# Optimization experiments

Hardware: AMD Instinct MI355X
Metric: run time of the kernel (lower is better)

## Reference

```python
import jax, jax.numpy as jnp
import numpy as np

B, T, C, D = 4, 2048, 48, 512
L = 16                    # transcript length per video (distinct labels)
K = 9                     # bdy_kernel
CS = 15                   # cs_kernel
N_TR = L - 1
N_CAND = 3 * N_TR         # candidate_mul * pt_num
WIN_LEN = int(T / L * 0.15)   # int(t / t_len * win_scale)
ALPHA, BETA, GAMMA, TEMP = 1.0, 1.0, 0.1, 0.1
LOG2 = float(np.log(2.0))

def _bdy_kernel():
    ker = np.zeros((K, K), np.float32)
    c = K // 2
    ker[:c, :c] = 1; ker[c:, c:] = 1
    ker[:c, c:] = -1; ker[c:, :c] = -1
    ker[c, c] = 0
    return jnp.asarray(ker)

BDY_KER = _bdy_kernel()

def bdy_score_fn(prob):
    # prob: [T, C]; sliding windows of size K over time (zero padded)
    c = K // 2
    pad = jnp.pad(prob, ((c, c), (0, 0)))
    win = pad[jnp.arange(T)[:, None] + jnp.arange(K)[None, :]]       # [T,K,C]
    p = win[:, :, None, :]                                           # [T,K,1,C]
    m = (p + win[:, None, :, :]) / 2                                 # [T,K,K,C]
    # torch F.kl_div((m+1e-32).log(), p) = p*(log p - log(m+1e-32)), xlogy(0)=0
    kl = jnp.sum(jnp.where(p > 0, p * (jnp.log(jnp.where(p > 0, p, 1.0)) - jnp.log(m + 1e-32)), 0.0), -1)
    js = (kl + jnp.swapaxes(kl, 1, 2)) / 2
    js = -(js / LOG2 * 2 - 1)                                        # [T,K,K]
    return jnp.mean(BDY_KER[None] * js, axis=(-1, -2))               # [T]

def dp(cls_score):
    # cls_score: [N_TR, N_CAND]; min-cost alignment DP, inner jj-loop vectorized
    cost = -cls_score
    n_tr, n_x = N_TR, N_CAND
    W = 2 * n_tr + 1
    col = jnp.arange(W)
    inf = jnp.float32(jnp.inf)
    tr_at = jnp.clip(col // 2, 0, n_tr - 1)
    even = (col % 2 == 0)
    ge2 = col >= 2

    def init_cols(ii):
        c0 = jnp.where(ii < n_x - n_tr, 0.0, inf)
        c1 = jnp.where(ii <= n_x - n_tr, cost[0, ii], inf)
        d1 = jnp.where(ii <= n_x - n_tr, 1, 0).astype(jnp.int32)
        return c0, c1, d1

    c0, c1, d1 = init_cols(0)
    row0 = jnp.full((W,), inf).at[0].set(c0).at[1].set(c1)
    dir0 = jnp.zeros((W,), jnp.int32).at[1].set(d1)

    def step(prev, ii):
        dm1 = jnp.concatenate([jnp.full((1,), inf), prev[:-1]])
        dm2 = jnp.concatenate([jnp.full((2,), inf), prev[:-2]])
        c_at = cost[:, ii][tr_at]
        even_val = jnp.minimum(prev, dm1)
        even_dir = jnp.where(prev < dm1, 0, 1).astype(jnp.int32)
        odd_val = c_at + jnp.minimum(dm1, dm2)
        odd_dir = jnp.where(dm1 < dm2, 1, 2).astype(jnp.int32)
        c0, c1, d1 = init_cols(ii)
        new = jnp.where(ge2, jnp.where(even, even_val, odd_val), inf)
        new = new.at[0].set(c0).at[1].set(c1)
        dirs = jnp.where(ge2, jnp.where(even, even_dir, odd_dir), 0).astype(jnp.int32)
        dirs = dirs.at[1].set(d1)
        return new, dirs

    last, dirs = jax.lax.scan(step, row0, jnp.arange(1, n_x))
    dir_mat = jnp.concatenate([dir0[None], dirs], 0)                 # [n_x, W]
    cur_j0 = jnp.where(last[2 * n_tr] < last[2 * n_tr - 1], 2 * n_tr, 2 * n_tr - 1).astype(jnp.int32)

    def bt(cur_j, x):
        ii, dir_row = x
        is_odd = (cur_j % 2) == 1
        out_idx = jnp.where(is_odd, cur_j // 2, jnp.int32(n_tr))     # n_tr = OOB -> dropped
        new_j = cur_j - dir_row[cur_j]
        return new_j, (out_idx, ii.astype(jnp.int32))

    _, (oi, ovals) = jax.lax.scan(bt, cur_j0, (jnp.arange(n_x), dir_mat), reverse=True)
    return jnp.zeros((n_tr,), jnp.int32).at[oi].set(ovals, mode='drop')

def detect(logit, tr):
    # logit: [T,C] (detached), tr: [L] ints -> boundary frame indices [N_TR]
    prob = jax.nn.softmax(logit, -1)
    score = bdy_score_fn(prob).at[0].set(-jnp.inf)
    backup = score
    pos = jnp.arange(T)

    def pick(s, _):
        i = jnp.argmax(s)
        return jnp.where(jnp.abs(pos - i) <= WIN_LEN, -jnp.inf, s), i

    _, cand = jax.lax.scan(pick, score, None, length=N_CAND)
    cand = jnp.sort(cand)                                            # [N_CAND]
    # class-transition score at candidate points
    cc = CS // 2
    pairs = jnp.pad(prob[:, tr], ((cc, cc), (0, 0)))                 # [T+2cc, L]
    win = pairs[cand[:, None] + jnp.arange(CS)[None, :]]             # [N_CAND, CS, L]
    first, second = win[:, :, :-1], win[:, :, 1:]
    k0 = jnp.where(jnp.arange(CS) < cc, 1.0, -1.0)[None, :, None]
    cls = jnp.sum(k0 * (first - second), axis=1) / (2 * CS)          # [N_CAND, N_TR]
    cls = cls.T + backup[cand][None, :]                              # [N_TR, N_CAND]
    return cand[dp(cls)]

def _forward(tok_logit, fr_logit, vid_multi_hot, feat, mask, transcript):
    y = vid_multi_hot
    tok_loss = jnp.mean(-(y * jax.nn.log_sigmoid(tok_logit) + (1 - y) * jax.nn.log_sigmoid(-tok_logit)))
    # boundary detection on detached logits
    bdy = jax.vmap(detect)(jax.lax.stop_gradient(fr_logit), transcript)   # [B, N_TR]
    pse = jax.vmap(lambda b, tr: tr[jnp.sum(jnp.arange(T)[:, None] >= b[None, :], axis=1)])(bdy, transcript)
    # frame CE (bgw==1.0 path, full mask so no -100 labels)
    logp = jax.nn.log_softmax(fr_logit, -1)
    ce = -jnp.take_along_axis(logp, pse[..., None], axis=-1)[..., 0]
    m = mask.astype(ce.dtype)
    fr_loss = jnp.sum(ce * m) / jnp.sum(m)
    # global-local contrast
    tok_feat = jax.lax.stop_gradient(feat[:, :C, :])
    fr_feat = feat[:, C:, :]

    def glc_one(tok, fr, pse_i, tr, m_i):
        labels = jnp.sort(tr)                                        # = unique(pse[mask]), distinct labels
        oh = (pse_i[None, :] == labels[:, None]).astype(fr.dtype) * m_i[None, :]
        cnt = jnp.maximum(jnp.sum(oh, 1, keepdims=True), 1.0)
        la = (oh @ fr) / cnt
        la = la / jnp.maximum(jnp.linalg.norm(la, axis=-1, keepdims=True), 1e-12)
        tk = tok / jnp.maximum(jnp.linalg.norm(tok, axis=-1, keepdims=True), 1e-12)
        sim = (la @ tk.T) / TEMP                                     # [L, C]
        return jnp.mean(-jnp.take_along_axis(jax.nn.log_softmax(sim, -1), labels[:, None], axis=-1))

    glc_loss = jnp.mean(jax.vmap(glc_one)(tok_feat, fr_feat, pse, transcript, mask.astype(feat.dtype)))
    return ALPHA * tok_loss + BETA * fr_loss + GAMMA * glc_loss

def setup_inputs() -> dict:
    key = jax.random.key(0)
    ks = jax.random.split(key, 5)
    tok_logit = jax.random.normal(ks[0], (B, C), jnp.float32)
    fr_logit = jax.random.normal(ks[1], (B, T, C), jnp.float32)
    mask = jnp.ones((B, T), bool)
    transcript = jax.vmap(lambda k: jax.random.permutation(k, C)[:L])(jax.random.split(ks[2], B)).astype(jnp.int32)
    vid_multi_hot = jax.random.uniform(ks[3], (B, C), jnp.float32)
    feat = jax.random.normal(ks[4], (B, C + T, D), jnp.float32)
    return {"epoch": 5, "tok_logit": tok_logit, "fr_logit": fr_logit, "mask": mask,
            "transcript": transcript, "vid_multi_hot": vid_multi_hot, "feat": feat}

def reference(epoch, tok_logit, fr_logit, mask, transcript, vid_multi_hot, feat):
    # epoch >= warm_epc (=0), so the full loss path runs
    return _forward(tok_logit, fr_logit, vid_multi_hot, feat, mask, transcript)
```

## Files before the change

kernel.cpp:

```cpp
#include <hip/hip_runtime.h>
#include <math.h>

#define BB 4
#define TT 2048
#define CC 48
#define DD 512
#define LL 16
#define NTR 15
#define NCAND 45
#define WINLEN 19
#define CSW 15
#define CCHALF 7

static __device__ __forceinline__ float wave_reduce_sum(float v) {
    for (int off = 32; off; off >>= 1) v += __shfl_down(v, off);
    return v;
}

#define DPPMAX(x, ctrl) fmaxf((x), __int_as_float(__builtin_amdgcn_update_dpp( \
    __float_as_int(x), __float_as_int(x), (ctrl), 0xF, 0xF, false)))

__global__ __launch_bounds__(256) void k_lse(const float* __restrict__ fr,
                                             float* __restrict__ lse) {
    int row = blockIdx.x * 4 + (threadIdx.x >> 6);
    int lane = threadIdx.x & 63;
    float xv = (lane < CC) ? fr[(size_t)row * CC + lane] : -INFINITY;
    float m = xv;
    for (int off = 32; off; off >>= 1) m = fmaxf(m, __shfl_down(m, off));
    m = __shfl(m, 0);
    float e = (lane < CC) ? __expf(xv - m) : 0.f;
    float s = wave_reduce_sum(e);
    if (lane == 0) lse[row] = m + __logf(s);
}

__global__ __launch_bounds__(64) void k_score(const float* __restrict__ fr,
                                              const float* __restrict__ lse,
                                              float* __restrict__ score) {
    int row = blockIdx.x;
    int b = row / TT, t = row % TT;
    __shared__ float sp[9][CC];
    __shared__ float slp[9][CC];
    __shared__ float lse_s[9];
    int tid = threadIdx.x;
    if (tid < 9) {
        int r = t - 4 + tid;
        lse_s[tid] = (r >= 0 && r < TT) ? lse[b * TT + r] : 0.f;
    }
    __syncthreads();
    for (int idx = tid; idx < 9 * CC; idx += 64) {
        int i = idx / CC, c = idx - (idx / CC) * CC;
        int r = t - 4 + i;
        float pv = 0.f, lv = 0.f;
        if (r >= 0 && r < TT) {
            float x = fr[((size_t)b * TT + r) * CC + c];
            lv = x - lse_s[i];
            pv = __expf(lv);
        }
        sp[i][c] = pv;
        slp[i][c] = lv;
    }
    __syncthreads();
    float acc = 0.f;
    for (int idx = tid; idx < 4 * CC; idx += 64) {
        int i = idx / CC, c = idx - (idx / CC) * CC;
        acc += -2.f * sp[i][c] * slp[i][c];
    }
    for (int item = tid; item < 36 * CC; item += 64) {
        int pidx = item / CC, c = item - pidx * CC;
        int i = 0, rem = pidx;
        while (rem >= 8 - i) { rem -= 8 - i; ++i; }
        int j = i + 1 + rem;
        float wgt = ((i < 4) == (j < 4)) ? 1.f : -1.f;
        float pi = sp[i][c], pj = sp[j][c];
        float logm = __logf(0.5f * (pi + pj) + 1e-32f);
        acc -= wgt * (pi + pj) * logm;
    }
    acc = wave_reduce_sum(acc);
    if (tid == 0) {
        const float SC = -2.0f / (81.0f * 0.6931471805599453f);
        score[row] = (t == 0) ? -INFINITY : SC * acc;
    }
}

__global__ __launch_bounds__(256) void k_pickdp(const float* __restrict__ fr,
                                                const float* __restrict__ lse,
                                                const float* __restrict__ score,
                                                const int* __restrict__ transcript,
                                                int* __restrict__ labels_out,
                                                int* __restrict__ pse,
                                                int* __restrict__ seg_start,
                                                int* __restrict__ seg_end) {
    int b = blockIdx.x;
    __shared__ float s[64 * 33];
    __shared__ int cl[NCAND];
    __shared__ float cost[NTR][NCAND];
    __shared__ int tr_s[LL];
    __shared__ int cand_s[NCAND];
    __shared__ float backup_s[NCAND];
    __shared__ signed char dir_mat[NCAND][32];
    __shared__ int bdy_s[NTR];
    __shared__ int rank_s[LL];
    int tid = threadIdx.x;
    if (tid < LL) tr_s[tid] = transcript[b * LL + tid];
    for (int t = tid; t < TT; t += 256) s[t + (t >> 5)] = score[(size_t)b * TT + t];
    __syncthreads();

    if (tid < 64) {
        int lane = tid;
        float v[32];
        #pragma unroll
        for (int k = 0; k < 32; ++k) v[k] = s[lane * 33 + k];
        int base = lane << 5;
        for (int it = 0; it < NCAND; ++it) {
            float best = -INFINITY; int bi = 0;
            #pragma unroll
            for (int k = 31; k >= 0; --k)
                if (v[k] >= best) { best = v[k]; bi = k; }
            float m = best;
            m = DPPMAX(m, 0x111); m = DPPMAX(m, 0x112);
            m = DPPMAX(m, 0x114); m = DPPMAX(m, 0x118);
            m = DPPMAX(m, 0x142); m = DPPMAX(m, 0x143);
            float gmax = __int_as_float(__builtin_amdgcn_readlane(__float_as_int(m), 63));
            unsigned long long ball = __ballot(best == gmax);
            int sl = (int)(__ffsll(ball) - 1);
            int mp = __builtin_amdgcn_readlane(base + bi, sl);
            if (lane == 0) cl[it] = mp;
            int llo = mp - WINLEN - base;
            int lhi = mp + WINLEN - base;
            unsigned lowm = (llo <= 0) ? 0xffffffffu : ((llo >= 32) ? 0u : ~((1u << llo) - 1u));
            unsigned him  = (lhi >= 31) ? 0xffffffffu : ((lhi < 0) ? 0u : ((2u << lhi) - 1u));
            unsigned wm = lowm & him;
            #pragma unroll
            for (int k = 0; k < 32; ++k)
                if (wm & (1u << k)) v[k] = -INFINITY;
        }
        if (lane < NCAND) {
            int my = cl[lane];
            int rank = 0;
            for (int i = 0; i < NCAND; ++i) rank += (cl[i] < my) ? 1 : 0;
            cand_s[rank] = my;
        }
    }
    __syncthreads();
    if (tid < NCAND) {
        int cp = cand_s[tid];
        backup_s[tid] = s[cp + (cp >> 5)];
    }
    __syncthreads();

    for (int e = tid; e < NTR * NCAND; e += 256) {
        int j = e / NCAND, ii = e - (e / NCAND) * NCAND;
        int cpos = cand_s[ii];
        int trj = tr_s[j], trj1 = tr_s[j + 1];
        float sum = 0.f;
        for (int k = 0; k < CSW; ++k) {
            int r = cpos - CCHALF + k;
            float a = 0.f, d2 = 0.f;
            if (r >= 0 && r < TT) {
                size_t ro = (size_t)b * TT + r;
                float ls = lse[ro];
                a  = __expf(fr[ro * CC + trj]  - ls);
                d2 = __expf(fr[ro * CC + trj1] - ls);
            }
            sum += ((k < CCHALF) ? 1.f : -1.f) * (a - d2);
        }
        cost[j][ii] = -(sum / 30.f + backup_s[ii]);
    }
    __syncthreads();

    if (tid < 64) {
        int lane = tid;
        float prev = INFINITY;
        if (lane == 0) prev = 0.f;
        if (lane == 1) prev = cost[0][0];
        if (lane < 31) dir_mat[0][lane] = (lane == 1) ? (signed char)1 : (signed char)0;
        for (int ii = 1; ii < NCAND; ++ii) {
            float dm1 = __shfl_up(prev, 1); if (lane < 1) dm1 = INFINITY;
            float dm2 = __shfl_up(prev, 2); if (lane < 2) dm2 = INFINITY;
            int trat = lane >> 1; if (trat > NTR - 1) trat = NTR - 1;
            float c_at = cost[trat][ii];
            float ev = fminf(prev, dm1);
            int ed = (prev < dm1) ? 0 : 1;
            float ov = c_at + fminf(dm1, dm2);
            int od = (dm1 < dm2) ? 1 : 2;
            float nv; int nd;
            if (lane >= 2) {
                if ((lane & 1) == 0) { nv = ev; nd = ed; }
                else { nv = ov; nd = od; }
            } else { nv = INFINITY; nd = 0; }
            if (lane == 0) { nv = (ii < NCAND - NTR) ? 0.f : INFINITY; nd = 0; }
            if (lane == 1) {
                nv = (ii <= NCAND - NTR) ? cost[0][ii] : INFINITY;
                nd = (ii <= NCAND - NTR) ? 1 : 0;
            }
            prev = nv;
            if (lane < 31) dir_mat[ii][lane] = (signed char)nd;
        }
        float v29 = __shfl(prev, 29);
        float v30 = __shfl(prev, 30);
        if (lane == 0) {
            int cur = (v30 < v29) ? 30 : 29;
            for (int ii = NCAND - 1; ii >= 0; --ii) {
                if (cur & 1) bdy_s[cur >> 1] = cand_s[ii];
                cur -= (int)dir_mat[ii][cur];
            }
            int lab[LL];
            for (int i2 = 0; i2 < LL; ++i2) lab[i2] = tr_s[i2];
            for (int a2 = 1; a2 < LL; ++a2) {
                int key = lab[a2]; int b2 = a2 - 1;
                while (b2 >= 0 && lab[b2] > key) { lab[b2 + 1] = lab[b2]; --b2; }
                lab[b2 + 1] = key;
            }
            for (int i2 = 0; i2 < LL; ++i2) labels_out[b * LL + i2] = lab[i2];
            for (int j2 = 0; j2 < LL; ++j2) {
                int r2 = 0;
                for (int l2 = 0; l2 < LL; ++l2) if (lab[l2] == tr_s[j2]) r2 = l2;
                rank_s[j2] = r2;
            }
            for (int j2 = 0; j2 < LL; ++j2) {
                int st = (j2 == 0) ? 0 : bdy_s[j2 - 1];
                int en = (j2 == LL - 1) ? TT : bdy_s[j2];
                seg_start[b * LL + rank_s[j2]] = st;
                seg_end[b * LL + rank_s[j2]] = en;
            }
        }
    }
    __syncthreads();
    for (int t = tid; t < TT; t += 256) {
        int cnt = 0;
        for (int j = 0; j < NTR; ++j) cnt += (t >= bdy_s[j]) ? 1 : 0;
        pse[b * TT + t] = tr_s[cnt];
    }
}

__global__ __launch_bounds__(256) void k_la(const float* __restrict__ feat,
                                            const int* __restrict__ seg_start,
                                            const int* __restrict__ seg_end,
                                            float* __restrict__ la) {
    int l = blockIdx.x, b = blockIdx.y;
    int st = seg_start[b * LL + l], en = seg_end[b * LL + l];
    int wave = threadIdx.x >> 6, lane = threadIdx.x & 63;
    const float* fr = feat + ((size_t)b * (CC + TT) + CC) * DD;
    __shared__ float part[4][DD];
    float4 a0 = {0,0,0,0}, a1 = {0,0,0,0};
    for (int r = st + wave; r < en; r += 4) {
        const float4* p = (const float4*)(fr + (size_t)r * DD);
        float4 v0 = p[lane];
        float4 v1 = p[64 + lane];
        a0.x += v0.x; a0.y += v0.y; a0.z += v0.z; a0.w += v0.w;
        a1.x += v1.x; a1.y += v1.y; a1.z += v1.z; a1.w += v1.w;
    }
    ((float4*)part[wave])[lane] = a0;
    ((float4*)part[wave])[64 + lane] = a1;
    __syncthreads();
    float* lar = la + ((size_t)b * LL + l) * DD;
    for (int idx = threadIdx.x; idx < DD; idx += 256)
        lar[idx] = part[0][idx] + part[1][idx] + part[2][idx] + part[3][idx];
}

__global__ __launch_bounds__(256) void k_glc(const float* __restrict__ feat,
                                             const float* __restrict__ la,
                                             const int* __restrict__ labels,
                                             float* __restrict__ terms) {
    int l = blockIdx.x, b = blockIdx.y;
    __shared__ float la_s[DD];
    __shared__ float sim_s[CC];
    __shared__ float red[4];
    __shared__ float s_inv_nla;
    int tid = threadIdx.x;
    int wave = tid >> 6, lane = tid & 63;
    const float* lar = la + ((size_t)b * LL + l) * DD;
    float2 lv = ((const float2*)lar)[tid];
    ((float2*)la_s)[tid] = lv;
    float ss = lv.x * lv.x + lv.y * lv.y;
    ss = wave_reduce_sum(ss);
    if (lane == 0) red[wave] = ss;
    __syncthreads();
    if (tid == 0)
        s_inv_nla = 10.0f / fmaxf(sqrtf(red[0] + red[1] + red[2] + red[3]), 1e-12f);
    __syncthreads();
    for (int c = wave; c < CC; c += 4) {
        const float4* tr = (const float4*)(feat + ((size_t)b * (CC + TT) + c) * DD);
        const float4* ls = (const float4*)la_s;
        float dot = 0.f, vv = 0.f;
        for (int j = lane; j < DD / 4; j += 64) {
            float4 a = ls[j]; float4 v = tr[j];
            dot += a.x * v.x + a.y * v.y + a.z * v.z + a.w * v.w;
            vv  += v.x * v.x + v.y * v.y + v.z * v.z + v.w * v.w;
        }
        dot = wave_reduce_sum(dot);
        vv  = wave_reduce_sum(vv);
        if (lane == 0)
            sim_s[c] = dot * s_inv_nla / fmaxf(sqrtf(vv), 1e-12f);
    }
    __syncthreads();
    if (tid == 0) {
        float mx = -INFINITY;
        for (int c = 0; c < CC; ++c) mx = fmaxf(mx, sim_s[c]);
        float se = 0.f;
        for (int c = 0; c < CC; ++c) se += expf(sim_s[c] - mx);
        int lab = labels[b * LL + l];
        terms[b * LL + l] = (mx + logf(se)) - sim_s[lab];
    }
}

__global__ __launch_bounds__(256) void k_fr(const float* __restrict__ fr_logit,
                                            const float* __restrict__ lse,
                                            const int* __restrict__ pse,
                                            float* __restrict__ fr_part) {
    __shared__ float red[4];
    int tid = threadIdx.x;
    float acc = 0.f;
    for (int k = 0; k < 4; ++k) {
        int i = blockIdx.x * 1024 + k * 256 + tid;
        int p = pse[i];
        acc += lse[i] - fr_logit[(size_t)i * CC + p];
    }
    acc = wave_reduce_sum(acc);
    if ((tid & 63) == 0) red[tid >> 6] = acc;
    __syncthreads();
    if (tid == 0) fr_part[blockIdx.x] = red[0] + red[1] + red[2] + red[3];
}

__global__ __launch_bounds__(256) void k_combine(const float* __restrict__ tok_logit,
                                                 const float* __restrict__ vid,
                                                 const float* __restrict__ fr_part,
                                                 const float* __restrict__ terms,
                                                 float* __restrict__ out) {
    int tid = threadIdx.x;
    __shared__ float red[4];
    float acc = 0.f;
    if (tid < BB * CC) {
        float x = tok_logit[tid], y = vid[tid];
        float lsp = fminf(x, 0.f) - log1pf(expf(-fabsf(x)));
        float lsn = fminf(-x, 0.f) - log1pf(expf(-fabsf(x)));
        acc = -(y * lsp + (1.f - y) * lsn);
    }
    float w = wave_reduce_sum(acc);
    if ((tid & 63) == 0) red[tid >> 6] = w;
    __syncthreads();
    if (tid == 0) {
        float s_tok = (red[0] + red[1] + red[2] + red[3]) / (float)(BB * CC);
        float sfr = 0.f;
        for (int i = 0; i < 8; ++i) sfr += fr_part[i];
        float s_fr = sfr / (float)(BB * TT);
        float g = 0.f;
        for (int i = 0; i < BB * LL; ++i) g += terms[i];
        float glc = g / (float)(BB * LL);
        out[0] = s_tok + s_fr + 0.1f * glc;
    }
}

extern "C" void kernel_launch(void* const* d_in, const int* in_sizes, int n_in,
                              void* d_out, int out_size, void* d_ws, size_t ws_size,
                              hipStream_t stream) {
    (void)in_sizes; (void)n_in; (void)out_size; (void)ws_size;
    const float* tok_logit  = (const float*)d_in[1];
    const float* fr_logit   = (const float*)d_in[2];
    const int*   transcript = (const int*)d_in[4];
    const float* vid        = (const float*)d_in[5];
    const float* feat       = (const float*)d_in[6];

    char* ws = (char*)d_ws;
    float* lse     = (float*)(ws + 0);
    float* score   = (float*)(ws + 32768);
    float* la      = (float*)(ws + 65536);
    float* terms   = (float*)(ws + 196608);
    float* fr_part = (float*)(ws + 196864);
    int*   labels  = (int*)(ws + 197120);
    int*   pse     = (int*)(ws + 197376);
    int*   seg_st  = (int*)(ws + 230144);
    int*   seg_en  = (int*)(ws + 230400);
    float* out     = (float*)d_out;

    k_lse<<<BB * TT / 4, 256, 0, stream>>>(fr_logit, lse);
    k_score<<<BB * TT, 64, 0, stream>>>(fr_logit, lse, score);
    k_pickdp<<<BB, 256, 0, stream>>>(fr_logit, lse, score, transcript,
                                     labels, pse, seg_st, seg_en);
    k_fr<<<8, 256, 0, stream>>>(fr_logit, lse, pse, fr_part);
    k_la<<<dim3(LL, BB), 256, 0, stream>>>(feat, seg_st, seg_en, la);
    k_glc<<<dim3(LL, BB), 256, 0, stream>>>(feat, la, labels, terms);
    k_combine<<<1, 256, 0, stream>>>(tok_logit, vid, fr_part, terms, out);
}
```

Baseline: 202.9 us.

## Fuse frame loss into pick/DP and merge segment-average with GLC kernel

The peak-picking loop in k_pickdp now spreads the score scan over all four waves instead of one. Each thread holds 8 values, and the waves combine their maxima through shared memory with a barrier per iteration. The frame cross-entropy is computed directly inside k_pickdp from the DP boundaries, which removes the pse buffer and the k_fr launch. k_la and k_glc are merged so the segment-average vector stays in shared memory. The goal is fewer kernel launches and less global traffic, at the cost of 45 block-wide barriers in the argmax loop.

```diff
diff --git a/kernel.cpp b/kernel.cpp
--- a/kernel.cpp
+++ b/kernel.cpp
@@ -87,11 +87,10 @@
                                                 const float* __restrict__ score,
                                                 const int* __restrict__ transcript,
                                                 int* __restrict__ labels_out,
-                                                int* __restrict__ pse,
                                                 int* __restrict__ seg_start,
-                                                int* __restrict__ seg_end) {
+                                                int* __restrict__ seg_end,
+                                                float* __restrict__ fr_part) {
     int b = blockIdx.x;
-    __shared__ float s[64 * 33];
     __shared__ int cl[NCAND];
     __shared__ float cost[NTR][NCAND];
     __shared__ int tr_s[LL];
@@ -100,52 +99,59 @@
     __shared__ signed char dir_mat[NCAND][32];
     __shared__ int bdy_s[NTR];
     __shared__ int rank_s[LL];
+    __shared__ float rv[2][4];
+    __shared__ int rp[2][4];
+    __shared__ float redf[4];
     int tid = threadIdx.x;
+    int wave = tid >> 6, lane = tid & 63;
     if (tid < LL) tr_s[tid] = transcript[b * LL + tid];
-    for (int t = tid; t < TT; t += 256) s[t + (t >> 5)] = score[(size_t)b * TT + t];
-    __syncthreads();
-
-    if (tid < 64) {
-        int lane = tid;
-        float v[32];
+
+    float v[8];
+    {
+        const float4* sp4 = (const float4*)(score + (size_t)b * TT);
+        float4 va = sp4[2 * tid], vb = sp4[2 * tid + 1];
+        v[0] = va.x; v[1] = va.y; v[2] = va.z; v[3] = va.w;
+        v[4] = vb.x; v[5] = vb.y; v[6] = vb.z; v[7] = vb.w;
+    }
+    for (int it = 0; it < NCAND; ++it) {
+        float best = -INFINITY; int bi = 0;
         #pragma unroll
-        for (int k = 0; k < 32; ++k) v[k] = s[lane * 33 + k];
-        int base = lane << 5;
-        for (int it = 0; it < NCAND; ++it) {
-            float best = -INFINITY; int bi = 0;
-            #pragma unroll
-            for (int k = 31; k >= 0; --k)
-                if (v[k] >= best) { best = v[k]; bi = k; }
-            float m = best;
-            m = DPPMAX(m, 0x111); m = DPPMAX(m, 0x112);
-            m = DPPMAX(m, 0x114); m = DPPMAX(m, 0x118);
-            m = DPPMAX(m, 0x142); m = DPPMAX(m, 0x143);
-            float gmax = __int_as_float(__builtin_amdgcn_readlane(__float_as_int(m), 63));
-            unsigned long long ball = __ballot(best == gmax);
-            int sl = (int)(__ffsll(ball) - 1);
-            int mp = __builtin_amdgcn_readlane(base + bi, sl);
-            if (lane == 0) cl[it] = mp;
-            int llo = mp - WINLEN - base;
-            int lhi = mp + WINLEN - base;
-            unsigned lowm = (llo <= 0) ? 0xffffffffu : ((llo >= 32) ? 0u : ~((1u << llo) - 1u));
-            unsigned him  = (lhi >= 31) ? 0xffffffffu : ((lhi < 0) ? 0u : ((2u << lhi) - 1u));
-            unsigned wm = lowm & him;
-            #pragma unroll
-            for (int k = 0; k < 32; ++k)
-                if (wm & (1u << k)) v[k] = -INFINITY;
-        }
-        if (lane < NCAND) {
-            int my = cl[lane];
-            int rank = 0;
-            for (int i = 0; i < NCAND; ++i) rank += (cl[i] < my) ? 1 : 0;
-            cand_s[rank] = my;
+        for (int k = 7; k >= 0; --k)
+            if (v[k] >= best) { best = v[k]; bi = k; }
+        int pos = tid * 8 + bi;
+        float m = best;
+        m = DPPMAX(m, 0x111); m = DPPMAX(m, 0x112);
+        m = DPPMAX(m, 0x114); m = DPPMAX(m, 0x118);
+        m = DPPMAX(m, 0x142); m = DPPMAX(m, 0x143);
+        float wmax = __int_as_float(__builtin_amdgcn_readlane(__float_as_int(m), 63));
+        unsigned long long ball = __ballot(best == wmax);
+        int sl = (int)(__ffsll((long long)ball) - 1);
+        int wpos = __builtin_amdgcn_readlane(pos, sl);
+        if (lane == 0) { rv[it & 1][wave] = wmax; rp[it & 1][wave] = wpos; }
+        __syncthreads();
+        float bvv = -INFINITY; int mp = 0x7fffffff;
+        #pragma unroll
+        for (int w = 0; w < 4; ++w) {
+            float vv = rv[it & 1][w]; int pp = rp[it & 1][w];
+            if (vv > bvv || (vv == bvv && pp < mp)) { bvv = vv; mp = pp; }
+        }
+        if (tid == 0) cl[it] = mp;
+        int lo = mp - WINLEN, hi = mp + WINLEN;
+        #pragma unroll
+        for (int k = 0; k < 8; ++k) {
+            int t = tid * 8 + k;
+            if (t >= lo && t <= hi) v[k] = -INFINITY;
         }
     }
     __syncthreads();
     if (tid < NCAND) {
-        int cp = cand_s[tid];
-        backup_s[tid] = s[cp + (cp >> 5)];
-    }
+        int my = cl[tid];
+        int rank = 0;
+        for (int i = 0; i < NCAND; ++i) rank += (cl[i] < my) ? 1 : 0;
+        cand_s[rank] = my;
+    }
+    __syncthreads();
+    if (tid < NCAND) backup_s[tid] = score[(size_t)b * TT + cand_s[tid]];
     __syncthreads();
 
     for (int e = tid; e < NTR * NCAND; e += 256) {
@@ -169,36 +175,35 @@
     __syncthreads();
 
     if (tid < 64) {
-        int lane = tid;
         float prev = INFINITY;
-        if (lane == 0) prev = 0.f;
-        if (lane == 1) prev = cost[0][0];
-        if (lane < 31) dir_mat[0][lane] = (lane == 1) ? (signed char)1 : (signed char)0;
+        if (tid == 0) prev = 0.f;
+        if (tid == 1) prev = cost[0][0];
+        if (tid < 31) dir_mat[0][tid] = (tid == 1) ? (signed char)1 : (signed char)0;
         for (int ii = 1; ii < NCAND; ++ii) {
-            float dm1 = __shfl_up(prev, 1); if (lane < 1) dm1 = INFINITY;
-            float dm2 = __shfl_up(prev, 2); if (lane < 2) dm2 = INFINITY;
-            int trat = lane >> 1; if (trat > NTR - 1) trat = NTR - 1;
+            float dm1 = __shfl_up(prev, 1); if (tid < 1) dm1 = INFINITY;
+            float dm2 = __shfl_up(prev, 2); if (tid < 2) dm2 = INFINITY;
+            int trat = tid >> 1; if (trat > NTR - 1) trat = NTR - 1;
             float c_at = cost[trat][ii];
             float ev = fminf(prev, dm1);
             int ed = (prev < dm1) ? 0 : 1;
             float ov = c_at + fminf(dm1, dm2);
             int od = (dm1 < dm2) ? 1 : 2;
             float nv; int nd;
-            if (lane >= 2) {
-                if ((lane & 1) == 0) { nv = ev; nd = ed; }
+            if (tid >= 2) {
+                if ((tid & 1) == 0) { nv = ev; nd = ed; }
                 else { nv = ov; nd = od; }
             } else { nv = INFINITY; nd = 0; }
-            if (lane == 0) { nv = (ii < NCAND - NTR) ? 0.f : INFINITY; nd = 0; }
-            if (lane == 1) {
+            if (tid == 0) { nv = (ii < NCAND - NTR) ? 0.f : INFINITY; nd = 0; }
+            if (tid == 1) {
                 nv = (ii <= NCAND - NTR) ? cost[0][ii] : INFINITY;
                 nd = (ii <= NCAND - NTR) ? 1 : 0;
             }
             prev = nv;
-            if (lane < 31) dir_mat[ii][lane] = (signed char)nd;
+            if (tid < 31) dir_mat[ii][tid] = (signed char)nd;
         }
         float v29 = __shfl(prev, 29);
         float v30 = __shfl(prev, 30);
-        if (lane == 0) {
+        if (tid == 0) {
             int cur = (v30 < v29) ? 30 : 29;
             for (int ii = NCAND - 1; ii >= 0; --ii) {
                 if (cur & 1) bdy_s[cur >> 1] = cand_s[ii];
@@ -226,25 +231,39 @@
         }
     }
     __syncthreads();
+
+    float facc = 0.f;
     for (int t = tid; t < TT; t += 256) {
         int cnt = 0;
         for (int j = 0; j < NTR; ++j) cnt += (t >= bdy_s[j]) ? 1 : 0;
-        pse[b * TT + t] = tr_s[cnt];
-    }
-}
-
-__global__ __launch_bounds__(256) void k_la(const float* __restrict__ feat,
-                                            const int* __restrict__ seg_start,
-                                            const int* __restrict__ seg_end,
-                                            float* __restrict__ la) {
+        int pv = tr_s[cnt];
+        size_t ro = (size_t)b * TT + t;
+        facc += lse[ro] - fr[ro * CC + pv];
+    }
+    facc = wave_reduce_sum(facc);
+    if (lane == 0) redf[wave] = facc;
+    __syncthreads();
+    if (tid == 0) fr_part[b] = redf[0] + redf[1] + redf[2] + redf[3];
+}
+
+__global__ __launch_bounds__(256) void k_laglc(const float* __restrict__ feat,
+                                               const int* __restrict__ seg_start,
+                                               const int* __restrict__ seg_end,
+                                               const int* __restrict__ labels,
+                                               float* __restrict__ terms) {
     int l = blockIdx.x, b = blockIdx.y;
     int st = seg_start[b * LL + l], en = seg_end[b * LL + l];
-    int wave = threadIdx.x >> 6, lane = threadIdx.x & 63;
-    const float* fr = feat + ((size_t)b * (CC + TT) + CC) * DD;
+    int tid = threadIdx.x;
+    int wave = tid >> 6, lane = tid & 63;
+    const float* frf = feat + ((size_t)b * (CC + TT) + CC) * DD;
     __shared__ float part[4][DD];
+    __shared__ float la_s[DD];
+    __shared__ float sim_s[CC];
+    __shared__ float red[4];
+    __shared__ float s_inv_nla;
     float4 a0 = {0,0,0,0}, a1 = {0,0,0,0};
     for (int r = st + wave; r < en; r += 4) {
-        const float4* p = (const float4*)(fr + (size_t)r * DD);
+        const float4* p = (const float4*)(frf + (size_t)r * DD);
         float4 v0 = p[lane];
         float4 v1 = p[64 + lane];
         a0.x += v0.x; a0.y += v0.y; a0.z += v0.z; a0.w += v0.w;
@@ -253,28 +272,14 @@
     ((float4*)part[wave])[lane] = a0;
     ((float4*)part[wave])[64 + lane] = a1;
     __syncthreads();
-    float* lar = la + ((size_t)b * LL + l) * DD;
-    for (int idx = threadIdx.x; idx < DD; idx += 256)
-        lar[idx] = part[0][idx] + part[1][idx] + part[2][idx] + part[3][idx];
-}
-
-__global__ __launch_bounds__(256) void k_glc(const float* __restrict__ feat,
-                                             const float* __restrict__ la,
-                                             const int* __restrict__ labels,
-                                             float* __restrict__ terms) {
-    int l = blockIdx.x, b = blockIdx.y;
-    __shared__ float la_s[DD];
-    __shared__ float sim_s[CC];
-    __shared__ float red[4];
-    __shared__ float s_inv_nla;
-    int tid = threadIdx.x;
-    int wave = tid >> 6, lane = tid & 63;
-    const float* lar = la + ((size_t)b * LL + l) * DD;
-    float2 lv = ((const float2*)lar)[tid];
-    ((float2*)la_s)[tid] = lv;
-    float ss = lv.x * lv.x + lv.y * lv.y;
-    ss = wave_reduce_sum(ss);
-    if (lane == 0) red[wave] = ss;
+    float ssl = 0.f;
+    for (int idx = tid; idx < DD; idx += 256) {
+        float s = part[0][idx] + part[1][idx] + part[2][idx] + part[3][idx];
+        la_s[idx] = s;
+        ssl += s * s;
+    }
+    ssl = wave_reduce_sum(ssl);
+    if (lane == 0) red[wave] = ssl;
     __syncthreads();
     if (tid == 0)
         s_inv_nla = 10.0f / fmaxf(sqrtf(red[0] + red[1] + red[2] + red[3]), 1e-12f);
@@ -284,9 +289,9 @@
         const float4* ls = (const float4*)la_s;
         float dot = 0.f, vv = 0.f;
         for (int j = lane; j < DD / 4; j += 64) {
-            float4 a = ls[j]; float4 v = tr[j];
-            dot += a.x * v.x + a.y * v.y + a.z * v.z + a.w * v.w;
-            vv  += v.x * v.x + v.y * v.y + v.z * v.z + v.w * v.w;
+            float4 a = ls[j]; float4 w = tr[j];
+            dot += a.x * w.x + a.y * w.y + a.z * w.z + a.w * w.w;
+            vv  += w.x * w.x + w.y * w.y + w.z * w.z + w.w * w.w;
         }
         dot = wave_reduce_sum(dot);
         vv  = wave_reduce_sum(vv);
@@ -302,24 +307,6 @@
         int lab = labels[b * LL + l];
         terms[b * LL + l] = (mx + logf(se)) - sim_s[lab];
     }
-}
-
-__global__ __launch_bounds__(256) void k_fr(const float* __restrict__ fr_logit,
-                                            const float* __restrict__ lse,
-                                            const int* __restrict__ pse,
-                                            float* __restrict__ fr_part) {
-    __shared__ float red[4];
-    int tid = threadIdx.x;
-    float acc = 0.f;
-    for (int k = 0; k < 4; ++k) {
-        int i = blockIdx.x * 1024 + k * 256 + tid;
-        int p = pse[i];
-        acc += lse[i] - fr_logit[(size_t)i * CC + p];
-    }
-    acc = wave_reduce_sum(acc);
-    if ((tid & 63) == 0) red[tid >> 6] = acc;
-    __syncthreads();
-    if (tid == 0) fr_part[blockIdx.x] = red[0] + red[1] + red[2] + red[3];
 }
 
 __global__ __launch_bounds__(256) void k_combine(const float* __restrict__ tok_logit,
@@ -341,8 +328,7 @@
     __syncthreads();
     if (tid == 0) {
         float s_tok = (red[0] + red[1] + red[2] + red[3]) / (float)(BB * CC);
-        float sfr = 0.f;
-        for (int i = 0; i < 8; ++i) sfr += fr_part[i];
+        float sfr = fr_part[0] + fr_part[1] + fr_part[2] + fr_part[3];
         float s_fr = sfr / (float)(BB * TT);
         float g = 0.f;
         for (int i = 0; i < BB * LL; ++i) g += terms[i];
@@ -364,21 +350,17 @@
     char* ws = (char*)d_ws;
     float* lse     = (float*)(ws + 0);
     float* score   = (float*)(ws + 32768);
-    float* la      = (float*)(ws + 65536);
-    float* terms   = (float*)(ws + 196608);
-    float* fr_part = (float*)(ws + 196864);
-    int*   labels  = (int*)(ws + 197120);
-    int*   pse     = (int*)(ws + 197376);
-    int*   seg_st  = (int*)(ws + 230144);
-    int*   seg_en  = (int*)(ws + 230400);
+    float* terms   = (float*)(ws + 65536);
+    float* fr_part = (float*)(ws + 65792);
+    int*   labels  = (int*)(ws + 66048);
+    int*   seg_st  = (int*)(ws + 66304);
+    int*   seg_en  = (int*)(ws + 66560);
     float* out     = (float*)d_out;
 
     k_lse<<<BB * TT / 4, 256, 0, stream>>>(fr_logit, lse);
     k_score<<<BB * TT, 64, 0, stream>>>(fr_logit, lse, score);
     k_pickdp<<<BB, 256, 0, stream>>>(fr_logit, lse, score, transcript,
-                                     labels, pse, seg_st, seg_en);
-    k_fr<<<8, 256, 0, stream>>>(fr_logit, lse, pse, fr_part);
-    k_la<<<dim3(LL, BB), 256, 0, stream>>>(feat, seg_st, seg_en, la);
-    k_glc<<<dim3(LL, BB), 256, 0, stream>>>(feat, la, labels, terms);
+                                     labels, seg_st, seg_en, fr_part);
+    k_laglc<<<dim3(LL, BB), 256, 0, stream>>>(feat, seg_st, seg_en, labels, terms);
     k_combine<<<1, 256, 0, stream>>>(tok_logit, vid, fr_part, terms, out);
 }
```

New measurement: 199.4 us. About the same (-1.8%).
